# Optimization experiments

Hardware: AMD Instinct MI355X
Metric: run time of the kernel (lower is better)

The kernel has to match this reference:

```python
import jax, jax.numpy as jnp
import numpy as np

BATCH, SEQ, IN_DIM = 4, 2048, 4
D_MODEL, HEADS, D_HEAD = 128, 8, 16
DEPTH, BUCKET, N_HASHES = 6, 64, 8
D_FF = 4 * D_MODEL
NUM_CLASSES = 2
NB = SEQ // BUCKET          # 32 buckets per hash round
SELF_ATTN_VALUE = -5e4      # lucidrains TOKEN_SELF_ATTN_VALUE


def setup_inputs() -> dict:
    key = jax.random.key(0)
    ks = jax.random.split(key, 12)
    rn = lambda k, s: jax.random.normal(k, s, jnp.float32) * 0.02
    return {
        "x": jax.random.normal(ks[0], (BATCH, SEQ, IN_DIM), jnp.float32),
        "emb_W": rn(ks[1], (IN_DIM, D_MODEL)),
        "emb_b": jnp.zeros((D_MODEL,), jnp.float32),
        "Wqk": rn(ks[2], (DEPTH, D_MODEL, D_MODEL)),
        "Wv": rn(ks[3], (DEPTH, D_MODEL, D_MODEL)),
        "Wo": rn(ks[4], (DEPTH, D_MODEL, D_MODEL)),
        "R": jax.random.normal(ks[5], (DEPTH, HEADS, D_HEAD, N_HASHES, NB // 2), jnp.float32),
        "ln1_g": jnp.ones((DEPTH, D_MODEL), jnp.float32),
        "ln1_b": jnp.zeros((DEPTH, D_MODEL), jnp.float32),
        "ln2_g": jnp.ones((DEPTH, D_MODEL), jnp.float32),
        "ln2_b": jnp.zeros((DEPTH, D_MODEL), jnp.float32),
        "ff_W1": rn(ks[6], (DEPTH, D_MODEL, D_FF)),
        "ff_b1": jnp.zeros((DEPTH, D_FF), jnp.float32),
        "ff_W2": rn(ks[7], (DEPTH, D_FF, D_MODEL)),
        "ff_b2": jnp.zeros((DEPTH, D_MODEL), jnp.float32),
        "fc_W": rn(ks[8], (D_MODEL, NUM_CLASSES)),
        "fc_b": jnp.zeros((NUM_CLASSES,), jnp.float32),
    }


def layer_norm(x, g, b, eps=1e-5):
    m = x.mean(-1, keepdims=True)
    v = ((x - m) ** 2).mean(-1, keepdims=True)
    return (x - m) * jax.lax.rsqrt(v + eps) * g + b


def lsh_attention(x, wqk, wv, wo, rot):
    # x: [B,S,D]; rot: [H, dh, n_hashes, NB//2]. Shared-QK LSH attention (eval mode, no dropout).
    B, S, D = x.shape
    qk = (x @ wqk).reshape(B, S, HEADS, D_HEAD).transpose(0, 2, 1, 3)  # [B,H,S,dh]
    v = (x @ wv).reshape(B, S, HEADS, D_HEAD).transpose(0, 2, 1, 3)

    # --- hashing: argmax over [xR; -xR] rotations ---
    rx = jnp.einsum('bhsd,hdnr->bhnsr', qk, rot)                # [B,H,n_hashes,S,NB/2]
    buckets = jnp.argmax(jnp.concatenate([rx, -rx], -1), -1)    # [B,H,n_hashes,S] in [0,NB)
    buckets = buckets + (jnp.arange(N_HASHES) * NB)[None, None, :, None]
    buckets = buckets.reshape(B, HEADS, N_HASHES * S)

    # --- stable sort by (bucket, position) ---
    ticker = jnp.arange(N_HASHES * S)
    sticker = jnp.argsort(buckets * S + (ticker % S), axis=-1)   # [B,H,L]
    undo = jnp.argsort(sticker, axis=-1)
    st = sticker % S                                              # original positions

    sqk = jnp.take_along_axis(qk, st[..., None], axis=2)          # [B,H,L,dh]
    sv = jnp.take_along_axis(v, st[..., None], axis=2)

    n_chunks = N_HASHES * NB
    bq = sqk.reshape(B, HEADS, n_chunks, BUCKET, D_HEAD)
    bk = bq / jnp.linalg.norm(bq, axis=-1, keepdims=True)         # shared-QK: keys are normalized queries
    bv = sv.reshape(B, HEADS, n_chunks, BUCKET, D_HEAD)
    bt = st.reshape(B, HEADS, n_chunks, BUCKET)

    look_back = lambda t: jnp.concatenate([t, jnp.roll(t, 1, axis=2)], axis=3)
    bk, bv, bkt = look_back(bk), look_back(bv), look_back(bt)

    dots = jnp.einsum('bhcid,bhcjd->bhcij', bq, bk) * (D_HEAD ** -0.5)  # [B,H,C,64,128]
    dots = jnp.where(bt[..., :, None] == bkt[..., None, :], SELF_ATTN_VALUE, dots)

    logsum = jax.nn.logsumexp(dots, axis=-1)                      # [B,H,C,64]
    probs = jnp.exp(dots - logsum[..., None])
    bo = jnp.einsum('bhcij,bhcjd->bhcid', probs, bv)

    so = bo.reshape(B, HEADS, N_HASHES * S, D_HEAD)
    slog = logsum.reshape(B, HEADS, N_HASHES * S)
    o = jnp.take_along_axis(so, undo[..., None], axis=2).reshape(B, HEADS, N_HASHES, S, D_HEAD)
    logits = jnp.take_along_axis(slog, undo, axis=2).reshape(B, HEADS, N_HASHES, S, 1)

    w = jax.nn.softmax(logits, axis=2)                            # combine hash rounds
    out = (o * w).sum(axis=2)                                     # [B,H,S,dh]
    out = out.transpose(0, 2, 1, 3).reshape(B, S, D)
    return out @ wo


def reference(x, emb_W, emb_b, Wqk, Wv, Wo, R, ln1_g, ln1_b, ln2_g, ln2_b,
              ff_W1, ff_b1, ff_W2, ff_b2, fc_W, fc_b):
    h = x @ emb_W + emb_b

    def layer(h, p):
        wqk, wv, wo, r, g1, b1g, g2, b2g, w1, bb1, w2, bb2 = p
        h = h + lsh_attention(layer_norm(h, g1, b1g), wqk, wv, wo, r)
        y = layer_norm(h, g2, b2g)
        h = h + (jax.nn.gelu(y @ w1 + bb1) @ w2 + bb2)
        return h, None

    h, _ = jax.lax.scan(layer, h, (Wqk, Wv, Wo, R, ln1_g, ln1_b, ln2_g, ln2_b,
                                   ff_W1, ff_b1, ff_W2, ff_b2))
    return h.mean(axis=1) @ fc_W + fc_b
```

## Files before the change

kernel.cpp:

```cpp
#include <hip/hip_runtime.h>
#include <math.h>

#define BB 4
#define SS 2048
#define INDIM 4
#define DD 128
#define HH 8
#define DH 16
#define DEPTH 6
#define BUCKET 64
#define NHASH 8
#define NBK 32
#define DFF 512
#define LL (NHASH*SS)
#define NCHUNK (NHASH*NBK)
#define NBH (BB*HH)

typedef short bf16x8 __attribute__((ext_vector_type(8)));
typedef _Float16 f16x8 __attribute__((ext_vector_type(8)));
typedef float f32x4 __attribute__((ext_vector_type(4)));

__device__ __forceinline__ unsigned short f2bf(float f) {
    unsigned u = __builtin_bit_cast(unsigned, f);
    unsigned r = u + 0x7FFFu + ((u >> 16) & 1u);
    return (unsigned short)(r >> 16);
}

__global__ void k_embed(const float* __restrict__ x, const float* __restrict__ W,
                        const float* __restrict__ b, float* __restrict__ h) {
    int idx = blockIdx.x * blockDim.x + threadIdx.x;
    if (idx >= BB*SS*DD) return;
    int d = idx % DD, bs = idx / DD;
    const float* xr = x + bs*INDIM;
    float acc = b[d];
    #pragma unroll
    for (int k = 0; k < INDIM; k++) acc += xr[k] * W[k*DD + d];
    h[idx] = acc;
}

__global__ void k_wcast(const float* __restrict__ src, unsigned short* __restrict__ dst,
                        int R, int C) {
    __shared__ float tile[32][33];
    int l = blockIdx.z;
    const float* s = src + (size_t)l*R*C;
    unsigned short* d = dst + (size_t)l*R*C;
    int c0 = blockIdx.x*32, r0 = blockIdx.y*32;
    int tx = threadIdx.x, ty = threadIdx.y;
    #pragma unroll
    for (int i = 0; i < 4; i++)
        tile[ty + i*8][tx] = s[(size_t)(r0 + ty + i*8)*C + c0 + tx];
    __syncthreads();
    #pragma unroll
    for (int i = 0; i < 4; i++)
        d[(size_t)(c0 + ty + i*8)*R + r0 + tx] = f2bf(tile[tx][ty + i*8]);
}

__global__ void k_wcast16(const float* __restrict__ src, _Float16* __restrict__ dst,
                          int R, int C) {
    __shared__ float tile[32][33];
    int l = blockIdx.z;
    const float* s = src + (size_t)l*R*C;
    _Float16* d = dst + (size_t)l*R*C;
    int c0 = blockIdx.x*32, r0 = blockIdx.y*32;
    int tx = threadIdx.x, ty = threadIdx.y;
    #pragma unroll
    for (int i = 0; i < 4; i++)
        tile[ty + i*8][tx] = s[(size_t)(r0 + ty + i*8)*C + c0 + tx];
    __syncthreads();
    #pragma unroll
    for (int i = 0; i < 4; i++)
        d[(size_t)(c0 + ty + i*8)*R + r0 + tx] = (_Float16)tile[tx][ty + i*8];
}

__global__ __launch_bounds__(256, 4)
void k_proj_qkv(const float* __restrict__ hin, const float* __restrict__ lng,
                const float* __restrict__ lnb, const _Float16* __restrict__ WqkT,
                const _Float16* __restrict__ WvT, float* __restrict__ qk,
                float* __restrict__ v) {
    __shared__ float A[16][128];
    __shared__ __align__(16) _Float16 Lf[16][136];
    int row0 = blockIdx.x * 16;
    int t = threadIdx.x;
    {
        const float4* src = (const float4*)(hin + (size_t)row0*DD);
        float4* dst = (float4*)&A[0][0];
        dst[t]       = src[t];
        dst[t + 256] = src[t + 256];
    }
    __syncthreads();
    {
        int r = t >> 4, sub = t & 15;
        float4 xa = *(const float4*)&A[r][sub*8];
        float4 xb = *(const float4*)&A[r][sub*8 + 4];
        float s = xa.x+xa.y+xa.z+xa.w + xb.x+xb.y+xb.z+xb.w;
        s += __shfl_xor(s,1); s += __shfl_xor(s,2);
        s += __shfl_xor(s,4); s += __shfl_xor(s,8);
        float m = s * (1.0f/128.0f);
        float d0=xa.x-m, d1=xa.y-m, d2=xa.z-m, d3=xa.w-m;
        float d4=xb.x-m, d5=xb.y-m, d6=xb.z-m, d7=xb.w-m;
        float vs = d0*d0+d1*d1+d2*d2+d3*d3+d4*d4+d5*d5+d6*d6+d7*d7;
        vs += __shfl_xor(vs,1); vs += __shfl_xor(vs,2);
        vs += __shfl_xor(vs,4); vs += __shfl_xor(vs,8);
        float inv = 1.0f / sqrtf(vs * (1.0f/128.0f) + 1e-5f);
        float4 ga = *(const float4*)&lng[sub*8], gb = *(const float4*)&lng[sub*8+4];
        float4 ba = *(const float4*)&lnb[sub*8], bb = *(const float4*)&lnb[sub*8+4];
        f16x8 vv;
        vv[0] = (_Float16)(d0*inv*ga.x + ba.x);
        vv[1] = (_Float16)(d1*inv*ga.y + ba.y);
        vv[2] = (_Float16)(d2*inv*ga.z + ba.z);
        vv[3] = (_Float16)(d3*inv*ga.w + ba.w);
        vv[4] = (_Float16)(d4*inv*gb.x + bb.x);
        vv[5] = (_Float16)(d5*inv*gb.y + bb.y);
        vv[6] = (_Float16)(d6*inv*gb.z + bb.z);
        vv[7] = (_Float16)(d7*inv*gb.w + bb.w);
        *(f16x8*)&Lf[r][sub*8] = vv;
    }
    __syncthreads();
    int w = t >> 6, lane = t & 63;
    int fr = lane & 15, kg = lane >> 4;
    f32x4 aq[2], av[2];
    aq[0] = (f32x4){0.f,0.f,0.f,0.f}; aq[1] = (f32x4){0.f,0.f,0.f,0.f};
    av[0] = (f32x4){0.f,0.f,0.f,0.f}; av[1] = (f32x4){0.f,0.f,0.f,0.f};
    #pragma unroll
    for (int ks = 0; ks < 4; ks++) {
        f16x8 af = *(const f16x8*)&Lf[fr][ks*32 + kg*8];
        #pragma unroll
        for (int nt = 0; nt < 2; nt++) {
            const _Float16* bp = WqkT + (size_t)(w*32 + nt*16 + fr)*128 + ks*32 + kg*8;
            f16x8 bq = *(const f16x8*)bp;
            aq[nt] = __builtin_amdgcn_mfma_f32_16x16x32_f16(af, bq, aq[nt], 0, 0, 0);
            const _Float16* vp = WvT + (size_t)(w*32 + nt*16 + fr)*128 + ks*32 + kg*8;
            f16x8 bv = *(const f16x8*)vp;
            av[nt] = __builtin_amdgcn_mfma_f32_16x16x32_f16(af, bv, av[nt], 0, 0, 0);
        }
    }
    int b = row0 / SS;
    int sb = row0 & (SS-1);
    #pragma unroll
    for (int nt = 0; nt < 2; nt++) {
        int n = w*32 + nt*16 + fr;
        int h_ = n >> 4, d_ = n & 15;
        #pragma unroll
        for (int i = 0; i < 4; i++) {
            int s = sb + kg*4 + i;
            size_t o = (((size_t)(b*HH + h_))*SS + s)*DH + d_;
            qk[o] = aq[nt][i]; v[o] = av[nt][i];
        }
    }
}

__global__ void k_hash(const float* __restrict__ qk, const float* __restrict__ R,
                       int* __restrict__ bkt) {
    __shared__ float Rs[256];
    int idx = blockIdx.x*256 + threadIdx.x;
    int s = idx & (SS-1); int t2 = idx >> 11;
    int n = t2 & 7; int bh = t2 >> 3; int h_ = bh & 7;
    {
        int tt = threadIdx.x;
        int d = tt >> 4, r = tt & 15;
        Rs[tt] = R[(((h_*DH + d)*NHASH + n)*16) + r];
    }
    __syncthreads();
    const float4* q4 = (const float4*)(qk + ((size_t)bh*SS + s)*DH);
    float4 q0 = q4[0], q1 = q4[1], q2 = q4[2], q3 = q4[3];
    float rxv[16];
    #pragma unroll
    for (int r = 0; r < 16; r++) {
        rxv[r] = q0.x*Rs[  0+r] + q0.y*Rs[ 16+r] + q0.z*Rs[ 32+r] + q0.w*Rs[ 48+r]
               + q1.x*Rs[ 64+r] + q1.y*Rs[ 80+r] + q1.z*Rs[ 96+r] + q1.w*Rs[112+r]
               + q2.x*Rs[128+r] + q2.y*Rs[144+r] + q2.z*Rs[160+r] + q2.w*Rs[176+r]
               + q3.x*Rs[192+r] + q3.y*Rs[208+r] + q3.z*Rs[224+r] + q3.w*Rs[240+r];
    }
    float best = rxv[0]; int bi = 0;
    #pragma unroll
    for (int jx = 1; jx < 16; jx++) if (rxv[jx]  > best) { best = rxv[jx];  bi = jx; }
    #pragma unroll
    for (int jx = 0; jx < 16; jx++) if (-rxv[jx] > best) { best = -rxv[jx]; bi = 16 + jx; }
    bkt[idx] = n*NBK + bi;
}

__global__ void k_scatter(const int* __restrict__ bkt, int* __restrict__ sticker) {
    __shared__ int hist[256*33];
    __shared__ int cs[8*33];
    __shared__ int bbk[NBK];
    int blk = blockIdx.x;
    int n = blk & 7, bh = blk >> 3;
    int t = threadIdx.x;
    #pragma unroll
    for (int k = 0; k < NBK; k++) hist[t*33 + k] = 0;
    const int* bp = bkt + (size_t)bh*LL + n*SS;
    int local[8];
    #pragma unroll
    for (int e = 0; e < 8; e++) {
        int k = bp[t*8 + e] - n*NBK;
        local[e] = k;
        hist[t*33 + k]++;
    }
    __syncthreads();
    {
        int i = t >> 5, k = t & 31;
        int ssum = 0;
        #pragma unroll
        for (int rr = 0; rr < 32; rr++) ssum += hist[(i*32+rr)*33 + k];
        cs[i*33 + k] = ssum;
    }
    __syncthreads();
    if (t < 32) {
        int tot = 0;
        #pragma unroll
        for (int i = 0; i < 8; i++) tot += cs[i*33 + t];
        int x = tot;
        #pragma unroll
        for (int o = 1; o < 32; o <<= 1) {
            int y = __shfl(x, (t >= o) ? (t - o) : 0, 64);
            if (t >= o) x += y;
        }
        bbk[t] = n*SS + x - tot;
    }
    __syncthreads();
    {
        int i = t >> 5, k = t & 31;
        int run = bbk[k];
        for (int ii = 0; ii < i; ii++) run += cs[ii*33 + k];
        for (int rr = 0; rr < 32; rr++) {
            int idx = (i*32+rr)*33 + k;
            int c0 = hist[idx];
            hist[idx] = run;
            run += c0;
        }
    }
    __syncthreads();
    #pragma unroll
    for (int e = 0; e < 8; e++) {
        int k = local[e];
        int pos = hist[t*33 + k]++;
        sticker[(size_t)bh*LL + pos] = n*SS + t*8 + e;
    }
}

__global__ __launch_bounds__(256, 3)
void k_attn(const float* __restrict__ qk, const float* __restrict__ v,
            const int* __restrict__ sticker, float* __restrict__ so,
            float* __restrict__ slog) {
    __shared__ __align__(16) char smem[33024];
    _Float16 (*Kf)[40]  = (_Float16(*)[40])smem;
    _Float16 (*P)[136]  = (_Float16(*)[136])(smem + 10240);
    _Float16 (*VT)[136] = (_Float16(*)[136])(smem + 27648);
    int*   pk   = (int*)(smem + 32000);
    float* nrm  = (float*)(smem + 32512);
    int*   lraw = (int*)(smem + 32768);

    int blk = blockIdx.x;
    int c = blk & (NCHUNK-1), bh = blk >> 8;
    int t = threadIdx.x;
    const int* stk = sticker + (size_t)bh*LL;
    const float4* qkb = (const float4*)(qk + (size_t)bh*SS*DH);
    const float4* vb  = (const float4*)(v  + (size_t)bh*SS*DH);

    if (t < 128) {
        int j = t;
        int cc = (j < 64) ? c : ((c + NCHUNK - 1) & (NCHUNK-1));
        int raw = stk[cc*BUCKET + (j & 63)];
        int sk = raw & (SS-1);
        float4 k0 = qkb[sk*4+0], k1 = qkb[sk*4+1], k2 = qkb[sk*4+2], k3 = qkb[sk*4+3];
        float ssq = k0.x*k0.x + k0.y*k0.y + k0.z*k0.z + k0.w*k0.w
                  + k1.x*k1.x + k1.y*k1.y + k1.z*k1.z + k1.w*k1.w
                  + k2.x*k2.x + k2.y*k2.y + k2.z*k2.z + k2.w*k2.w
                  + k3.x*k3.x + k3.y*k3.y + k3.z*k3.z + k3.w*k3.w;
        float nn = sqrtf(ssq);
        float inv = 1.0f / nn;
        f16x8 z = {0,0,0,0,0,0,0,0};
        f16x8 kf0, kf1;
        kf0[0]=(_Float16)(k0.x*inv); kf0[1]=(_Float16)(k0.y*inv);
        kf0[2]=(_Float16)(k0.z*inv); kf0[3]=(_Float16)(k0.w*inv);
        kf0[4]=(_Float16)(k1.x*inv); kf0[5]=(_Float16)(k1.y*inv);
        kf0[6]=(_Float16)(k1.z*inv); kf0[7]=(_Float16)(k1.w*inv);
        kf1[0]=(_Float16)(k2.x*inv); kf1[1]=(_Float16)(k2.y*inv);
        kf1[2]=(_Float16)(k2.z*inv); kf1[3]=(_Float16)(k2.w*inv);
        kf1[4]=(_Float16)(k3.x*inv); kf1[5]=(_Float16)(k3.y*inv);
        kf1[6]=(_Float16)(k3.z*inv); kf1[7]=(_Float16)(k3.w*inv);
        *(f16x8*)&Kf[j][0]  = kf0; *(f16x8*)&Kf[j][8]  = kf1;
        *(f16x8*)&Kf[j][16] = z;   *(f16x8*)&Kf[j][24] = z;
        pk[j] = sk;
        if (j < 64) { nrm[j] = nn * 0.25f; lraw[j] = raw; }
    } else {
        int j = t - 128;
        int cc = (j < 64) ? c : ((c + NCHUNK - 1) & (NCHUNK-1));
        int sk = stk[cc*BUCKET + (j & 63)] & (SS-1);
        float4 v0 = vb[sk*4+0], v1 = vb[sk*4+1], v2 = vb[sk*4+2], v3 = vb[sk*4+3];
        VT[ 0][j]=(_Float16)v0.x; VT[ 1][j]=(_Float16)v0.y;
        VT[ 2][j]=(_Float16)v0.z; VT[ 3][j]=(_Float16)v0.w;
        VT[ 4][j]=(_Float16)v1.x; VT[ 5][j]=(_Float16)v1.y;
        VT[ 6][j]=(_Float16)v1.z; VT[ 7][j]=(_Float16)v1.w;
        VT[ 8][j]=(_Float16)v2.x; VT[ 9][j]=(_Float16)v2.y;
        VT[10][j]=(_Float16)v2.z; VT[11][j]=(_Float16)v2.w;
        VT[12][j]=(_Float16)v3.x; VT[13][j]=(_Float16)v3.y;
        VT[14][j]=(_Float16)v3.z; VT[15][j]=(_Float16)v3.w;
    }
    __syncthreads();

    int w = t >> 6, lane = t & 63;
    int fr = lane & 15, kg = lane >> 4;
    int qrow = w*16 + fr;

    f32x4 acc[8];
    #pragma unroll
    for (int nt = 0; nt < 8; nt++) acc[nt] = (f32x4){0.f,0.f,0.f,0.f};
    {
        f16x8 kfq = *(const f16x8*)&Kf[qrow][kg*8];
        _Float16 qs = (_Float16)nrm[qrow];
        f16x8 a0 = kfq * qs;
        #pragma unroll
        for (int nt = 0; nt < 8; nt++) {
            f16x8 bfr = *(const f16x8*)&Kf[nt*16 + fr][kg*8];
            acc[nt] = __builtin_amdgcn_mfma_f32_16x16x32_f16(a0, bfr, acc[nt], 0, 0, 0);
        }
    }
    int pq[4], lr[4];
    #pragma unroll
    for (int i = 0; i < 4; i++) {
        int r = w*16 + kg*4 + i;
        pq[i] = pk[r]; lr[i] = lraw[r];
    }
    float s[4] = {0.f, 0.f, 0.f, 0.f};
    #pragma unroll
    for (int nt = 0; nt < 8; nt++) {
        int pkk = pk[nt*16 + fr];
        #pragma unroll
        for (int i = 0; i < 4; i++) {
            float d = acc[nt][i];
            d = (pq[i] == pkk) ? -5e4f : d;
            float p = __expf(d);
            s[i] += p;
            P[w*16 + kg*4 + i][nt*16 + fr] = (_Float16)p;
        }
    }
    #pragma unroll
    for (int i = 0; i < 4; i++) {
        s[i] += __shfl_xor(s[i], 1); s[i] += __shfl_xor(s[i], 2);
        s[i] += __shfl_xor(s[i], 4); s[i] += __shfl_xor(s[i], 8);
    }

    f32x4 oacc = (f32x4){0.f,0.f,0.f,0.f};
    #pragma unroll
    for (int ks = 0; ks < 4; ks++) {
        f16x8 af = *(const f16x8*)&P[w*16 + fr][ks*32 + kg*8];
        f16x8 bf = *(const f16x8*)&VT[fr][ks*32 + kg*8];
        oacc = __builtin_amdgcn_mfma_f32_16x16x32_f16(af, bf, oacc, 0, 0, 0);
    }
    #pragma unroll
    for (int i = 0; i < 4; i++) {
        float invs = 1.0f / s[i];
        int l = lr[i];
        so[((size_t)bh*LL + l)*DH + fr] = oacc[i] * invs;
        if (fr == 0) slog[(size_t)bh*LL + l] = __logf(s[i]);
    }
}

__global__ __launch_bounds__(256, 2)
void k_out_ffn(const float* __restrict__ so, const float* __restrict__ slog,
               const _Float16* __restrict__ WoT, const float* __restrict__ lng,
               const float* __restrict__ lnb, const unsigned short* __restrict__ W1T,
               const float* __restrict__ b1, const unsigned short* __restrict__ W2T,
               const float* __restrict__ b2, float* __restrict__ h) {
    __shared__ float hs[16][128];
    __shared__ __align__(16) _Float16 At[16][136];
    __shared__ __align__(16) unsigned short Albf[16][136];
    __shared__ __align__(16) unsigned short albf[16][520];
    int row0 = blockIdx.x * 16;
    int t = threadIdx.x;
    int b = row0 / SS;
    int s0 = row0 & (SS-1);

    {
        const float4* src = (const float4*)(h + (size_t)row0*DD);
        float4* dst = (float4*)&hs[0][0];
        dst[t]       = src[t];
        dst[t + 256] = src[t + 256];
    }
    {
        int half = t & 1, task = t >> 1;
        int r = task >> 3, h_ = task & 7;
        int s = s0 + r;
        int bh = b*HH + h_;
        const float* sl = slog + (size_t)bh*LL + s;
        float lg[NHASH];
        float m = -3.4e38f;
        #pragma unroll
        for (int n = 0; n < NHASH; n++) {
            lg[n] = sl[n*SS];
            m = fmaxf(m, lg[n]);
        }
        float sum = 0.f;
        #pragma unroll
        for (int n = 0; n < NHASH; n++) { lg[n] = __expf(lg[n] - m); sum += lg[n]; }
        float inv = 1.0f / sum;
        float4 o0 = {0,0,0,0}, o1 = {0,0,0,0};
        #pragma unroll
        for (int n = 0; n < NHASH; n++) {
            float wgt = lg[n]*inv;
            const float4* sp = (const float4*)(so + ((size_t)bh*LL + n*SS + s)*DH + half*8);
            float4 a = sp[0], bq = sp[1];
            o0.x += wgt*a.x;  o0.y += wgt*a.y;  o0.z += wgt*a.z;  o0.w += wgt*a.w;
            o1.x += wgt*bq.x; o1.y += wgt*bq.y; o1.z += wgt*bq.z; o1.w += wgt*bq.w;
        }
        f16x8 ov;
        ov[0]=(_Float16)o0.x; ov[1]=(_Float16)o0.y; ov[2]=(_Float16)o0.z; ov[3]=(_Float16)o0.w;
        ov[4]=(_Float16)o1.x; ov[5]=(_Float16)o1.y; ov[6]=(_Float16)o1.z; ov[7]=(_Float16)o1.w;
        *(f16x8*)&At[r][h_*16 + half*8] = ov;
    }
    __syncthreads();

    int w = t >> 6, lane = t & 63;
    int fr = lane & 15, kg = lane >> 4;

    {
        f32x4 ao[2];
        ao[0] = (f32x4){0.f,0.f,0.f,0.f}; ao[1] = (f32x4){0.f,0.f,0.f,0.f};
        #pragma unroll
        for (int ks = 0; ks < 4; ks++) {
            f16x8 af = *(const f16x8*)&At[fr][ks*32 + kg*8];
            #pragma unroll
            for (int nt = 0; nt < 2; nt++) {
                const _Float16* bp = WoT + (size_t)(w*32 + nt*16 + fr)*128 + ks*32 + kg*8;
                f16x8 bf = *(const f16x8*)bp;
                ao[nt] = __builtin_amdgcn_mfma_f32_16x16x32_f16(af, bf, ao[nt], 0, 0, 0);
            }
        }
        #pragma unroll
        for (int nt = 0; nt < 2; nt++)
            #pragma unroll
            for (int i = 0; i < 4; i++)
                hs[kg*4 + i][w*32 + nt*16 + fr] += ao[nt][i];
    }
    __syncthreads();

    {
        int r = t >> 4, sub = t & 15;
        float4 xa = *(const float4*)&hs[r][sub*8];
        float4 xb = *(const float4*)&hs[r][sub*8 + 4];
        float s = xa.x+xa.y+xa.z+xa.w + xb.x+xb.y+xb.z+xb.w;
        s += __shfl_xor(s,1); s += __shfl_xor(s,2);
        s += __shfl_xor(s,4); s += __shfl_xor(s,8);
        float m = s * (1.0f/128.0f);
        float d0=xa.x-m, d1=xa.y-m, d2=xa.z-m, d3=xa.w-m;
        float d4=xb.x-m, d5=xb.y-m, d6=xb.z-m, d7=xb.w-m;
        float vs = d0*d0+d1*d1+d2*d2+d3*d3+d4*d4+d5*d5+d6*d6+d7*d7;
        vs += __shfl_xor(vs,1); vs += __shfl_xor(vs,2);
        vs += __shfl_xor(vs,4); vs += __shfl_xor(vs,8);
        float inv = 1.0f / sqrtf(vs * (1.0f/128.0f) + 1e-5f);
        float4 ga = *(const float4*)&lng[sub*8], gb = *(const float4*)&lng[sub*8+4];
        float4 ba = *(const float4*)&lnb[sub*8], bb = *(const float4*)&lnb[sub*8+4];
        bf16x8 vv;
        vv[0] = (short)f2bf(d0*inv*ga.x + ba.x);
        vv[1] = (short)f2bf(d1*inv*ga.y + ba.y);
        vv[2] = (short)f2bf(d2*inv*ga.z + ba.z);
        vv[3] = (short)f2bf(d3*inv*ga.w + ba.w);
        vv[4] = (short)f2bf(d4*inv*gb.x + bb.x);
        vv[5] = (short)f2bf(d5*inv*gb.y + bb.y);
        vv[6] = (short)f2bf(d6*inv*gb.z + bb.z);
        vv[7] = (short)f2bf(d7*inv*gb.w + bb.w);
        *(bf16x8*)&Albf[r][sub*8] = vv;
    }
    __syncthreads();

    f32x4 acc1[8];
    #pragma unroll
    for (int i = 0; i < 8; i++) acc1[i] = (f32x4){0.f, 0.f, 0.f, 0.f};
    {
        const unsigned short* w1p = W1T + (size_t)(w*128 + fr)*128 + kg*8;
        #pragma unroll
        for (int ks = 0; ks < 4; ks++) {
            bf16x8 af = *(const bf16x8*)&Albf[fr][ks*32 + kg*8];
            #pragma unroll
            for (int nt = 0; nt < 8; nt++) {
                bf16x8 bf = *(const bf16x8*)(w1p + nt*16*128 + ks*32);
                acc1[nt] = __builtin_amdgcn_mfma_f32_16x16x32_bf16(af, bf, acc1[nt], 0, 0, 0);
            }
        }
    }
    #pragma unroll
    for (int nt = 0; nt < 8; nt++) {
        int col = w*128 + nt*16 + fr;
        float bias = b1[col];
        #pragma unroll
        for (int i = 0; i < 4; i++) {
            int row = kg*4 + i;
            float x = acc1[nt][i] + bias;
            float t0 = tanhf(0.7978845608028654f * (x + 0.044715f*x*x*x));
            albf[row][col] = f2bf(0.5f*x*(1.0f + t0));
        }
    }
    __syncthreads();

    f32x4 acc2[2];
    acc2[0] = (f32x4){0.f,0.f,0.f,0.f};
    acc2[1] = (f32x4){0.f,0.f,0.f,0.f};
    {
        const unsigned short* w2p = W2T + (size_t)(w*32 + fr)*512 + kg*8;
        #pragma unroll
        for (int ks = 0; ks < 16; ks++) {
            bf16x8 af = *(const bf16x8*)&albf[fr][ks*32 + kg*8];
            bf16x8 b0 = *(const bf16x8*)(w2p + ks*32);
            bf16x8 b1f = *(const bf16x8*)(w2p + 16*512 + ks*32);
            acc2[0] = __builtin_amdgcn_mfma_f32_16x16x32_bf16(af, b0, acc2[0], 0, 0, 0);
            acc2[1] = __builtin_amdgcn_mfma_f32_16x16x32_bf16(af, b1f, acc2[1], 0, 0, 0);
        }
    }
    #pragma unroll
    for (int nt = 0; nt < 2; nt++) {
        int col = w*32 + nt*16 + fr;
        float bias = b2[col];
        #pragma unroll
        for (int i = 0; i < 4; i++) {
            int row = kg*4 + i;
            h[(size_t)(row0 + row)*DD + col] = hs[row][col] + acc2[nt][i] + bias;
        }
    }
}

__global__ void k_pool(const float* __restrict__ h, float* __restrict__ partial) {
    int blk = blockIdx.x;
    int t = threadIdx.x;
    int b = blk >> 6, c = blk & 63;
    const float* hp = h + ((size_t)b*SS + c*32)*DD + t;
    float acc = 0.f;
    #pragma unroll
    for (int i = 0; i < 32; i++) acc += hp[i*DD];
    partial[blk*DD + t] = acc;
}

__global__ void k_final(const float* __restrict__ partial, const float* __restrict__ fcW,
                        const float* __restrict__ fcb, float* __restrict__ out) {
    __shared__ float red[4];
    int b = blockIdx.x, t = threadIdx.x;
    const float* pp = partial + (size_t)b*64*DD + t;
    float acc = 0.f;
    #pragma unroll
    for (int c = 0; c < 64; c++) acc += pp[c*DD];
    float pooled = acc * (1.0f/(float)SS);
    float p0 = pooled * fcW[t*2+0];
    float p1 = pooled * fcW[t*2+1];
    #pragma unroll
    for (int o = 32; o >= 1; o >>= 1) { p0 += __shfl_xor(p0,o); p1 += __shfl_xor(p1,o); }
    int w = t >> 6;
    if ((t & 63) == 0) { red[w*2] = p0; red[w*2+1] = p1; }
    __syncthreads();
    if (t == 0) {
        out[b*2 + 0] = red[0] + red[2] + fcb[0];
        out[b*2 + 1] = red[1] + red[3] + fcb[1];
    }
}

extern "C" void kernel_launch(void* const* d_in, const int* in_sizes, int n_in,
                              void* d_out, int out_size, void* d_ws, size_t ws_size,
                              hipStream_t stream) {
    const float* x    = (const float*)d_in[0];
    const float* embW = (const float*)d_in[1];
    const float* embB = (const float*)d_in[2];
    const float* Wqk  = (const float*)d_in[3];
    const float* Wv   = (const float*)d_in[4];
    const float* Wo   = (const float*)d_in[5];
    const float* R    = (const float*)d_in[6];
    const float* ln1g = (const float*)d_in[7];
    const float* ln1b = (const float*)d_in[8];
    const float* ln2g = (const float*)d_in[9];
    const float* ln2b = (const float*)d_in[10];
    const float* W1   = (const float*)d_in[11];
    const float* b1   = (const float*)d_in[12];
    const float* W2   = (const float*)d_in[13];
    const float* b2   = (const float*)d_in[14];
    const float* fcW  = (const float*)d_in[15];
    const float* fcb  = (const float*)d_in[16];
    float* out = (float*)d_out;

    char* w = (char*)d_ws;
    auto carve = [&](size_t bytes) -> char* {
        char* p = w;
        w += (bytes + 255) & ~(size_t)255;
        return p;
    };
    float* h       = (float*)carve((size_t)BB*SS*DD*4);
    float* qk      = (float*)carve((size_t)NBH*SS*DH*4);
    float* v       = (float*)carve((size_t)NBH*SS*DH*4);
    int*   bkt     = (int*)  carve((size_t)NBH*LL*4);
    int*   sticker = (int*)  carve((size_t)NBH*LL*4);
    float* so      = (float*)carve((size_t)NBH*LL*DH*4);
    float* slog    = (float*)carve((size_t)NBH*LL*4);
    float* partial = (float*)carve((size_t)BB*64*DD*4);
    unsigned short* w1t = (unsigned short*)carve((size_t)DEPTH*DD*DFF*2);
    unsigned short* w2t = (unsigned short*)carve((size_t)DEPTH*DFF*DD*2);
    _Float16* wqk16 = (_Float16*)carve((size_t)DEPTH*DD*DD*2);
    _Float16* wv16  = (_Float16*)carve((size_t)DEPTH*DD*DD*2);
    _Float16* wo16  = (_Float16*)carve((size_t)DEPTH*DD*DD*2);

    k_wcast<<<dim3(DFF/32, DD/32, DEPTH), dim3(32, 8), 0, stream>>>(W1, w1t, DD, DFF);
    k_wcast<<<dim3(DD/32, DFF/32, DEPTH), dim3(32, 8), 0, stream>>>(W2, w2t, DFF, DD);
    k_wcast16<<<dim3(DD/32, DD/32, DEPTH), dim3(32, 8), 0, stream>>>(Wqk, wqk16, DD, DD);
    k_wcast16<<<dim3(DD/32, DD/32, DEPTH), dim3(32, 8), 0, stream>>>(Wv, wv16, DD, DD);
    k_wcast16<<<dim3(DD/32, DD/32, DEPTH), dim3(32, 8), 0, stream>>>(Wo, wo16, DD, DD);

    k_embed<<<(BB*SS*DD)/256, 256, 0, stream>>>(x, embW, embB, h);

    for (int l = 0; l < DEPTH; l++) {
        const _Float16* wqkl = wqk16 + (size_t)l*DD*DD;
        const _Float16* wvl  = wv16  + (size_t)l*DD*DD;
        const _Float16* wol  = wo16  + (size_t)l*DD*DD;
        const float* rl  = R   + (size_t)l*HH*DH*NHASH*16;
        const float* g1  = ln1g + l*DD; const float* bg1 = ln1b + l*DD;
        const float* g2  = ln2g + l*DD; const float* bg2 = ln2b + l*DD;
        const unsigned short* w1l = w1t + (size_t)l*DD*DFF;
        const unsigned short* w2l = w2t + (size_t)l*DFF*DD;
        const float* bb1 = b1 + l*DFF;
        const float* bb2 = b2 + l*DD;

        k_proj_qkv<<<(BB*SS)/16, 256, 0, stream>>>(h, g1, bg1, wqkl, wvl, qk, v);
        k_hash<<<(NBH*NHASH*SS)/256, 256, 0, stream>>>(qk, rl, bkt);
        k_scatter<<<NBH*NHASH, 256, 0, stream>>>(bkt, sticker);
        k_attn<<<NBH*NCHUNK, 256, 0, stream>>>(qk, v, sticker, so, slog);
        k_out_ffn<<<(BB*SS)/16, 256, 0, stream>>>(so, slog, wol, g2, bg2,
                                                  w1l, bb1, w2l, bb2, h);
    }

    k_pool<<<BB*64, 128, 0, stream>>>(h, partial);
    k_final<<<BB, 128, 0, stream>>>(partial, fcW, fcb, out);
}
```

Measured before the change: 554.4 us.

## Fuse LSH hashing into QKV projection and store attention output in fp16

Hashing moves into the QKV projection kernel. The projected qk rows are staged in shared memory and bucketed there, which removes the separate k_hash launch and its re-read of qk from global memory. The per-hash-round attention output buffer changes from fp32 to fp16, halving its write traffic in k_attn and its read traffic in k_out_ffn, at some cost in precision. k_attn launch bounds rise from 3 to 4 blocks per CU. The fused hash reads R straight from global memory instead of through shared memory, and adds shared memory and work to the projection kernel.

```diff
diff --git a/kernel.cpp b/kernel.cpp
--- a/kernel.cpp
+++ b/kernel.cpp
@@ -75,10 +75,12 @@
 __global__ __launch_bounds__(256, 4)
 void k_proj_qkv(const float* __restrict__ hin, const float* __restrict__ lng,
                 const float* __restrict__ lnb, const _Float16* __restrict__ WqkT,
-                const _Float16* __restrict__ WvT, float* __restrict__ qk,
-                float* __restrict__ v) {
+                const _Float16* __restrict__ WvT, const float* __restrict__ Rl,
+                float* __restrict__ qk, float* __restrict__ v,
+                int* __restrict__ bkt) {
     __shared__ float A[16][128];
     __shared__ __align__(16) _Float16 Lf[16][136];
+    __shared__ float qs[16][132];
     int row0 = blockIdx.x * 16;
     int t = threadIdx.x;
     {
@@ -145,38 +147,41 @@
             int s = sb + kg*4 + i;
             size_t o = (((size_t)(b*HH + h_))*SS + s)*DH + d_;
             qk[o] = aq[nt][i]; v[o] = av[nt][i];
-        }
-    }
-}
-
-__global__ void k_hash(const float* __restrict__ qk, const float* __restrict__ R,
-                       int* __restrict__ bkt) {
-    __shared__ float Rs[256];
-    int idx = blockIdx.x*256 + threadIdx.x;
-    int s = idx & (SS-1); int t2 = idx >> 11;
-    int n = t2 & 7; int bh = t2 >> 3; int h_ = bh & 7;
-    {
-        int tt = threadIdx.x;
-        int d = tt >> 4, r = tt & 15;
-        Rs[tt] = R[(((h_*DH + d)*NHASH + n)*16) + r];
-    }
-    __syncthreads();
-    const float4* q4 = (const float4*)(qk + ((size_t)bh*SS + s)*DH);
-    float4 q0 = q4[0], q1 = q4[1], q2 = q4[2], q3 = q4[3];
-    float rxv[16];
-    #pragma unroll
-    for (int r = 0; r < 16; r++) {
-        rxv[r] = q0.x*Rs[  0+r] + q0.y*Rs[ 16+r] + q0.z*Rs[ 32+r] + q0.w*Rs[ 48+r]
-               + q1.x*Rs[ 64+r] + q1.y*Rs[ 80+r] + q1.z*Rs[ 96+r] + q1.w*Rs[112+r]
-               + q2.x*Rs[128+r] + q2.y*Rs[144+r] + q2.z*Rs[160+r] + q2.w*Rs[176+r]
-               + q3.x*Rs[192+r] + q3.y*Rs[208+r] + q3.z*Rs[224+r] + q3.w*Rs[240+r];
-    }
-    float best = rxv[0]; int bi = 0;
-    #pragma unroll
-    for (int jx = 1; jx < 16; jx++) if (rxv[jx]  > best) { best = rxv[jx];  bi = jx; }
-    #pragma unroll
-    for (int jx = 0; jx < 16; jx++) if (-rxv[jx] > best) { best = -rxv[jx]; bi = 16 + jx; }
-    bkt[idx] = n*NBK + bi;
+            qs[kg*4 + i][n] = aq[nt][i];
+        }
+    }
+    __syncthreads();
+    {
+        int r = t >> 4;
+        int h_ = (t >> 1) & 7;
+        int n0 = (t & 1) * 4;
+        int s = sb + r;
+        int bh = b*HH + h_;
+        float q[16];
+        #pragma unroll
+        for (int d = 0; d < 16; d++) q[d] = qs[r][h_*16 + d];
+        #pragma unroll
+        for (int nn = 0; nn < 4; nn++) {
+            int n = n0 + nn;
+            const float* Rp = Rl + ((size_t)(h_*DH)*NHASH + n)*16;
+            float rxv[16];
+            #pragma unroll
+            for (int j = 0; j < 16; j++) rxv[j] = 0.f;
+            #pragma unroll
+            for (int d = 0; d < 16; d++) {
+                float qd = q[d];
+                const float* rw = Rp + d*(NHASH*16);
+                #pragma unroll
+                for (int j = 0; j < 16; j++) rxv[j] += qd * rw[j];
+            }
+            float best = rxv[0]; int bi = 0;
+            #pragma unroll
+            for (int jx = 1; jx < 16; jx++) if (rxv[jx]  > best) { best = rxv[jx];  bi = jx; }
+            #pragma unroll
+            for (int jx = 0; jx < 16; jx++) if (-rxv[jx] > best) { best = -rxv[jx]; bi = 16 + jx; }
+            bkt[(size_t)bh*LL + n*SS + s] = n*NBK + bi;
+        }
+    }
 }
 
 __global__ void k_scatter(const int* __restrict__ bkt, int* __restrict__ sticker) {
@@ -238,9 +243,9 @@
     }
 }
 
-__global__ __launch_bounds__(256, 3)
+__global__ __launch_bounds__(256, 4)
 void k_attn(const float* __restrict__ qk, const float* __restrict__ v,
-            const int* __restrict__ sticker, float* __restrict__ so,
+            const int* __restrict__ sticker, _Float16* __restrict__ so,
             float* __restrict__ slog) {
     __shared__ __align__(16) char smem[33024];
     _Float16 (*Kf)[40]  = (_Float16(*)[40])smem;
@@ -352,13 +357,13 @@
     for (int i = 0; i < 4; i++) {
         float invs = 1.0f / s[i];
         int l = lr[i];
-        so[((size_t)bh*LL + l)*DH + fr] = oacc[i] * invs;
+        so[((size_t)bh*LL + l)*DH + fr] = (_Float16)(oacc[i] * invs);
         if (fr == 0) slog[(size_t)bh*LL + l] = __logf(s[i]);
     }
 }
 
 __global__ __launch_bounds__(256, 2)
-void k_out_ffn(const float* __restrict__ so, const float* __restrict__ slog,
+void k_out_ffn(const _Float16* __restrict__ so, const float* __restrict__ slog,
                const _Float16* __restrict__ WoT, const float* __restrict__ lng,
                const float* __restrict__ lnb, const unsigned short* __restrict__ W1T,
                const float* __restrict__ b1, const unsigned short* __restrict__ W2T,
@@ -395,18 +400,18 @@
         #pragma unroll
         for (int n = 0; n < NHASH; n++) { lg[n] = __expf(lg[n] - m); sum += lg[n]; }
         float inv = 1.0f / sum;
-        float4 o0 = {0,0,0,0}, o1 = {0,0,0,0};
+        float o[8] = {0,0,0,0,0,0,0,0};
         #pragma unroll
         for (int n = 0; n < NHASH; n++) {
             float wgt = lg[n]*inv;
-            const float4* sp = (const float4*)(so + ((size_t)bh*LL + n*SS + s)*DH + half*8);
-            float4 a = sp[0], bq = sp[1];
-            o0.x += wgt*a.x;  o0.y += wgt*a.y;  o0.z += wgt*a.z;  o0.w += wgt*a.w;
-            o1.x += wgt*bq.x; o1.y += wgt*bq.y; o1.z += wgt*bq.z; o1.w += wgt*bq.w;
+            const f16x8* sp = (const f16x8*)(so + ((size_t)bh*LL + n*SS + s)*DH + half*8);
+            f16x8 a = *sp;
+            #pragma unroll
+            for (int j = 0; j < 8; j++) o[j] += wgt*(float)a[j];
         }
         f16x8 ov;
-        ov[0]=(_Float16)o0.x; ov[1]=(_Float16)o0.y; ov[2]=(_Float16)o0.z; ov[3]=(_Float16)o0.w;
-        ov[4]=(_Float16)o1.x; ov[5]=(_Float16)o1.y; ov[6]=(_Float16)o1.z; ov[7]=(_Float16)o1.w;
+        #pragma unroll
+        for (int j = 0; j < 8; j++) ov[j] = (_Float16)o[j];
         *(f16x8*)&At[r][h_*16 + half*8] = ov;
     }
     __syncthreads();
@@ -585,7 +590,7 @@
     float* v       = (float*)carve((size_t)NBH*SS*DH*4);
     int*   bkt     = (int*)  carve((size_t)NBH*LL*4);
     int*   sticker = (int*)  carve((size_t)NBH*LL*4);
-    float* so      = (float*)carve((size_t)NBH*LL*DH*4);
+    _Float16* so   = (_Float16*)carve((size_t)NBH*LL*DH*2);
     float* slog    = (float*)carve((size_t)NBH*LL*4);
     float* partial = (float*)carve((size_t)BB*64*DD*4);
     unsigned short* w1t = (unsigned short*)carve((size_t)DEPTH*DD*DFF*2);
@@ -614,8 +619,7 @@
         const float* bb1 = b1 + l*DFF;
         const float* bb2 = b2 + l*DD;
 
-        k_proj_qkv<<<(BB*SS)/16, 256, 0, stream>>>(h, g1, bg1, wqkl, wvl, qk, v);
-        k_hash<<<(NBH*NHASH*SS)/256, 256, 0, stream>>>(qk, rl, bkt);
+        k_proj_qkv<<<(BB*SS)/16, 256, 0, stream>>>(h, g1, bg1, wqkl, wvl, rl, qk, v, bkt);
         k_scatter<<<NBH*NHASH, 256, 0, stream>>>(bkt, sticker);
         k_attn<<<NBH*NCHUNK, 256, 0, stream>>>(qk, v, sticker, so, slog);
         k_out_ffn<<<(BB*SS)/16, 256, 0, stream>>>(so, slog, wol, g2, bg2,
```

Result: slower. 837.7 us (+51.1%).
